# Optimization experiments

Hardware: AMD Instinct MI355X
Metric: run time of the kernel (lower is better)

The kernel has to match this reference:

```python
import jax, jax.numpy as jnp
import numpy as np

DIM = 1024
HID = 2816  # int(2*4096/3)=2730 rounded up to multiple of 256
E = 2       # n_modalities
N = 32768   # tokens
EPS = 1e-5


def setup_inputs() -> dict:
    key = jax.random.key(0)
    ks = jax.random.split(key, 6)
    x = jax.random.normal(ks[0], (N, DIM), jnp.float32)
    # per-token modality label -> disjoint boolean masks [E, N]
    labels = jax.random.randint(ks[1], (N,), 0, E)
    modality_masks = labels[None, :] == jnp.arange(E)[:, None]
    s_in = 1.0 / np.sqrt(DIM)
    s_hid = 1.0 / np.sqrt(HID)
    # nn.Linear stores weight as [out_features, in_features]
    w1 = jax.random.normal(ks[2], (E, HID, DIM), jnp.float32) * s_in
    w3 = jax.random.normal(ks[3], (E, HID, DIM), jnp.float32) * s_in
    w2 = jax.random.normal(ks[4], (E, DIM, HID), jnp.float32) * s_hid
    norm_w = jnp.ones((E, DIM), jnp.float32)
    return {"x": x, "modality_masks": modality_masks,
            "w1": w1, "w3": w3, "w2": w2, "norm_w": norm_w}


def reference(x, modality_masks, w1, w3, w2, norm_w):
    # Each expert: SwiGLU FFN followed by RMSNorm (computed in fp32).
    def expert(W1, W3, W2, g):
        h = jax.nn.silu(x @ W1.T) * (x @ W3.T)   # [N, HID]
        o = h @ W2.T                              # [N, DIM]
        of = o.astype(jnp.float32)
        n = of * jax.lax.rsqrt(jnp.mean(of * of, axis=-1, keepdims=True) + EPS)
        return (n * g.astype(jnp.float32)).astype(o.dtype)

    outs = jax.vmap(expert)(w1, w3, w2, norm_w)   # [E, N, DIM]
    merged = jnp.zeros_like(x)
    for i in range(E - 1, -1, -1):
        merged = jnp.where(modality_masks[i][:, None], outs[i], merged)
    return merged
```

## Files before the change

kernel.cpp:

```cpp
#include <hip/hip_runtime.h>
#include <stdint.h>

#define DIM   1024
#define HID   2816
#define NEXP  2
#define NTOK  32768
#define RMS_EPS 1e-5f
#define NK1   16
#define NK2   44
#define NNT1  22
#define NNT2  4

typedef unsigned short u16;
typedef unsigned int   u32;
typedef __bf16 bf16_t;
typedef bf16_t bf16x8 __attribute__((ext_vector_type(8)));
typedef float  f32x4  __attribute__((ext_vector_type(4)));
typedef float  f32x4v __attribute__((ext_vector_type(4)));

#define BAR() asm volatile("s_barrier" ::: "memory")
#define WAIT6() asm volatile("s_waitcnt vmcnt(6)" ::: "memory")
#define WAIT0() asm volatile("s_waitcnt vmcnt(0)" ::: "memory")
#define MFMA_(a,b,c) __builtin_amdgcn_mfma_f32_16x16x32_bf16(a, b, c, 0, 0, 0)

__device__ __forceinline__ u16 f2bf(float f) {
  u32 u = __float_as_uint(f);
  u += 0x7FFFu + ((u >> 16) & 1u);
  return (u16)(u >> 16);
}

__device__ __forceinline__ void gld16(void* lds, const void* g) {
  __builtin_amdgcn_global_load_lds(
      (__attribute__((address_space(1))) void*)g,
      (__attribute__((address_space(3))) void*)lds, 16, 0, 0);
}

__device__ __forceinline__ int detect_layout(const u32* mi) {
  const int lane = threadIdx.x & 63;
  bool all01 = true, allf = true;
  for (int j = 0; j < 8; ++j) {
    u32 w = mi[j * 64 + lane];
    all01 &= (w <= 1u);
    allf  &= (w == 0u || w == 0x3F800000u);
  }
  unsigned long long b01 = __ballot(all01);
  unsigned long long bfl = __ballot(allf);
  if (b01 == ~0ull) return 0;
  if (bfl == ~0ull) return 1;
  return 2;
}

__device__ __forceinline__ bool mask_at(const void* m, int layout, int e, int n) {
  if (layout == 0) return ((const u32*)m)[e * NTOK + n] != 0u;
  if (layout == 1) return ((const float*)m)[e * NTOK + n] != 0.f;
  return ((const unsigned char*)m)[e * NTOK + n] != 0;
}

__device__ __forceinline__ int label_of(const void* m, int layout, int n) {
  for (int e = 0; e < NEXP; ++e)
    if (mask_at(m, layout, e, n)) return e;
  return 0;
}

__global__ __launch_bounds__(1024) void k_setup(const void* __restrict__ masks,
                                                int* __restrict__ meta,
                                                int* __restrict__ idx) {
  const int layout = detect_layout((const u32*)masks);
  const int t = threadIdx.x;
  const int base_n = t << 5;
  u32 bits = 0; int c0 = 0;
  for (int j = 0; j < 32; ++j) {
    const int l_ = label_of(masks, layout, base_n + j);
    bits |= ((u32)l_) << j;
    c0 += 1 - l_;
  }
  int inc = c0;
#pragma unroll
  for (int d = 1; d < 64; d <<= 1) {
    int v = __shfl_up(inc, d, 64);
    if ((t & 63) >= d) inc += v;
  }
  __shared__ int wsum[16];
  __shared__ int wexc[17];
  const int wv = t >> 6;
  if ((t & 63) == 63) wsum[wv] = inc;
  __syncthreads();
  if (t == 0) {
    int a = 0;
    for (int w = 0; w < 16; ++w) { wexc[w] = a; a += wsum[w]; }
    wexc[16] = a;
  }
  __syncthreads();
  const int cnt0 = wexc[16];
  int p0 = wexc[wv] + inc - c0;
  int p1 = cnt0 + base_n - p0;
  for (int j = 0; j < 32; ++j) {
    const int n = base_n + j;
    if ((bits >> j) & 1u) idx[p1++] = n;
    else                  idx[p0++] = n;
  }
  if (t == 0) { meta[0] = cnt0; meta[1] = NTOK - cnt0; }
}

__global__ void k_cvtw(const float* __restrict__ w1, const float* __restrict__ w3,
                       const float* __restrict__ w2, u16* __restrict__ w1b,
                       u16* __restrict__ w3b, u16* __restrict__ w2b, int n4) {
  const int stride = gridDim.x * blockDim.x;
  for (int i = blockIdx.x * blockDim.x + threadIdx.x; i < 3 * n4; i += stride) {
    const f32x4v* src; ushort4* dst; int j;
    if (i < n4)            { src = (const f32x4v*)w1; dst = (ushort4*)w1b; j = i; }
    else if (i < 2 * n4)   { src = (const f32x4v*)w3; dst = (ushort4*)w3b; j = i - n4; }
    else                   { src = (const f32x4v*)w2; dst = (ushort4*)w2b; j = i - 2 * n4; }
    const f32x4v v = __builtin_nontemporal_load(&src[j]);
    ushort4 o;
    o.x = f2bf(v[0]); o.y = f2bf(v[1]); o.z = f2bf(v[2]); o.w = f2bf(v[3]);
    dst[j] = o;
  }
}

__global__ __launch_bounds__(256) void k_cvtx(const float* __restrict__ x,
                                              const int* __restrict__ idx,
                                              u16* __restrict__ xg) {
  const int r = blockIdx.x;
  const int tok = idx[r];
  const f32x4v v = __builtin_nontemporal_load(
      &((const f32x4v*)(x + ((size_t)tok << 10)))[threadIdx.x]);
  ushort4 o;
  o.x = f2bf(v[0]); o.y = f2bf(v[1]); o.z = f2bf(v[2]); o.w = f2bf(v[3]);
  ((ushort4*)(xg + ((size_t)r << 10)))[threadIdx.x] = o;
}


#define ST1A(BUF, HH, P_, KT) {                                        \
    char* _d = (char*)&sA[BUF][(HH) * 8192] + t * 16;                  \
    gld16(_d,        ((HH) ? P_.a2 : P_.a0) + (size_t)(KT) * 64);      \
    gld16(_d + 8192, ((HH) ? P_.a3 : P_.a1) + (size_t)(KT) * 64); }

#define ST1B(BUF, HH, P_, KT) {                                                 \
    gld16((char*)&sB1[BUF][(HH) * 4096] + t * 16,                               \
          ((HH) ? P_.b11 : P_.b10) + (size_t)(KT) * 64);                        \
    gld16((char*)&sB3[BUF][(HH) * 4096] + t * 16,                               \
          ((HH) ? P_.b31 : P_.b30) + (size_t)(KT) * 64); }

#define G1_PH(MQ, NQ, ...) {                                                   \
    if ((NQ) == 0) {                                                           \
      _Pragma("unroll") for (int mi = 0; mi < 4; ++mi) {                       \
        af0[mi] = *(const bf16x8*)&sAc[aBase + (MQ)*8192 + mi*1024 + kb0];     \
        af1[mi] = *(const bf16x8*)&sAc[aBase + (MQ)*8192 + mi*1024 + kb1];     \
      }                                                                        \
    }                                                                          \
    b1f0 = *(const bf16x8*)&sB1c[bBase + (NQ)*4096 + kb0];                     \
    b1f1 = *(const bf16x8*)&sB1c[bBase + (NQ)*4096 + kb1];                     \
    b3f0 = *(const bf16x8*)&sB3c[bBase + (NQ)*4096 + kb0];                     \
    b3f1 = *(const bf16x8*)&sB3c[bBase + (NQ)*4096 + kb1];                     \
    __VA_ARGS__                                                                \
    BAR();                                                                     \
    __builtin_amdgcn_s_setprio(1);                                             \
    _Pragma("unroll") for (int mi = 0; mi < 4; ++mi) {                         \
      acc1[MQ][NQ][mi] = MFMA_(af0[mi], b1f0, acc1[MQ][NQ][mi]);               \
      acc3[MQ][NQ][mi] = MFMA_(af0[mi], b3f0, acc3[MQ][NQ][mi]);               \
      acc1[MQ][NQ][mi] = MFMA_(af1[mi], b1f1, acc1[MQ][NQ][mi]);               \
      acc3[MQ][NQ][mi] = MFMA_(af1[mi], b3f1, acc3[MQ][NQ][mi]);               \
    }                                                                          \
    __builtin_amdgcn_s_setprio(0);                                             \
  }

#define SETUP1(P_, IT) {                                                        \
    int _it = (IT);                                                            \
    int _nt = _it / mcnt;                                                      \
    int _j  = _it - _nt * mcnt;                                                \
    int _m  = c + (_j << 3);                                                   \
    P_.nT   = _nt;                                                             \
    int _e  = _m >= nmt0;                                                      \
    P_.mT   = _e ? _m - nmt0 : _m;                                             \
    P_.cnt  = _e ? cnt1 : cnt0;                                                \
    P_.bas  = _e ? cnt0 : 0;                                                   \
    int _rg;                                                                   \
    _rg = P_.mT*256       + r0; _rg = _rg < P_.cnt ? _rg : P_.cnt-1;           \
    P_.a0 = xg + (size_t)(P_.bas+_rg)*DIM + srcoff;                            \
    _rg = P_.mT*256 +  64 + r0; _rg = _rg < P_.cnt ? _rg : P_.cnt-1;           \
    P_.a1 = xg + (size_t)(P_.bas+_rg)*DIM + srcoff;                            \
    _rg = P_.mT*256 + 128 + r0; _rg = _rg < P_.cnt ? _rg : P_.cnt-1;           \
    P_.a2 = xg + (size_t)(P_.bas+_rg)*DIM + srcoff;                            \
    _rg = P_.mT*256 + 192 + r0; _rg = _rg < P_.cnt ? _rg : P_.cnt-1;           \
    P_.a3 = xg + (size_t)(P_.bas+_rg)*DIM + srcoff;                            \
    size_t _o = ((size_t)_e * HID + (size_t)P_.nT * 128 + r0) * DIM + srcoff;  \
    P_.b10 = w1b + _o; P_.b11 = w1b + _o + (size_t)64 * DIM;                   \
    P_.b30 = w3b + _o; P_.b31 = w3b + _o + (size_t)64 * DIM; }

__global__ __launch_bounds__(512, 1) void k_gemm1(
    const u16* __restrict__ xg, const u16* __restrict__ w1b,
    const u16* __restrict__ w3b, const int* __restrict__ meta,
    u16* __restrict__ h)
{
  const int cnt0 = meta[0], cnt1 = meta[1];
  const int nmt0 = (cnt0 + 255) >> 8;
  const int nmt  = nmt0 + ((cnt1 + 255) >> 8);
  const int c = blockIdx.x & 7, q = blockIdx.x >> 3;
  const int mcnt  = (nmt > c) ? (((nmt - 1 - c) >> 3) + 1) : 0;
  const int items = mcnt * NNT1;
  int i = q;
  if (i >= items) return;

  __shared__ __attribute__((aligned(16))) u16 sA [2][256 * 64];
  __shared__ __attribute__((aligned(16))) u16 sB1[2][128 * 64];
  __shared__ __attribute__((aligned(16))) u16 sB3[2][128 * 64];

  const int t = threadIdx.x;
  const int srcoff = ((t & 7) ^ ((t >> 3) & 7)) * 8;
  const int r0 = t >> 3;
  const int wid = t >> 6, l = t & 63;
  const int wr = wid >> 2, wc = wid & 3;
  const int l15 = l & 15, lk = l >> 4, l7 = l & 7;
  const int kb0 = ((0 + lk) ^ l7) * 8;
  const int kb1 = ((4 + lk) ^ l7) * 8;
  const int aBase = (wr * 64 + l15) * 64;
  const int bBase = (wc * 16 + l15) * 64;

  struct P { const u16 *a0,*a1,*a2,*a3,*b10,*b11,*b30,*b31; int mT,cnt,bas,nT; };
  P cur, nxt;
  SETUP1(cur, i)
  bool hasN = (i + 32) < items;
  if (hasN) { SETUP1(nxt, i + 32) } else { nxt = cur; }

  f32x4 acc1[2][2][4] = {};
  f32x4 acc3[2][2][4] = {};
  bf16x8 af0[4], af1[4], b1f0, b1f1, b3f0, b3f1;

  ST1A(0, 0, cur, 0) ST1A(0, 1, cur, 0) ST1B(0, 0, cur, 0) ST1B(0, 1, cur, 0)
  ST1A(1, 0, cur, 1) ST1A(1, 1, cur, 1) ST1B(1, 0, cur, 1)
  WAIT6();
  BAR();

  for (;;) {
#pragma unroll 2
    for (int k = 0; k < NK1 - 2; ++k) {
      const u16* sAc  = &sA [k & 1][0];
      const u16* sB1c = &sB1[k & 1][0];
      const u16* sB3c = &sB3[k & 1][0];
      G1_PH(0, 0, ST1B((k & 1) ^ 1, 1, cur, k + 1))
      BAR();
      G1_PH(0, 1, ST1A(k & 1, 0, cur, k + 2))
      BAR();
      G1_PH(1, 0, )
      BAR();
      G1_PH(1, 1, ST1A(k & 1, 1, cur, k + 2) ST1B(k & 1, 0, cur, k + 2))
      WAIT6();
      BAR();
    }
    {
      const u16* sAc  = &sA [0][0];
      const u16* sB1c = &sB1[0][0];
      const u16* sB3c = &sB3[0][0];
      G1_PH(0, 0, ST1B(1, 1, cur, 15))
      BAR();
      G1_PH(0, 1, if (hasN) ST1A(0, 0, nxt, 0))
      BAR();
      G1_PH(1, 0, )
      BAR();
      G1_PH(1, 1, if (hasN) { ST1A(0, 1, nxt, 0) ST1B(0, 0, nxt, 0) })
      if (hasN) WAIT6(); else WAIT0();
      BAR();
    }
    {
      const u16* sAc  = &sA [1][0];
      const u16* sB1c = &sB1[1][0];
      const u16* sB3c = &sB3[1][0];
      G1_PH(0, 0, if (hasN) ST1B(0, 1, nxt, 0))
      BAR();
      G1_PH(0, 1, if (hasN) ST1A(1, 0, nxt, 1))
      BAR();
      G1_PH(1, 0, )
      BAR();
      G1_PH(1, 1, if (hasN) { ST1A(1, 1, nxt, 1) ST1B(1, 0, nxt, 1) })
      if (hasN) WAIT6();
      BAR();
    }

#pragma unroll
    for (int mq = 0; mq < 2; ++mq)
#pragma unroll
      for (int mi = 0; mi < 4; ++mi)
#pragma unroll
        for (int r = 0; r < 4; ++r) {
          const int lrow = mq * 128 + wr * 64 + mi * 16 + lk * 4 + r;
          const int rg = cur.mT * 256 + lrow;
          if (rg < cur.cnt) {
            u16* hrow = h + (size_t)(cur.bas + rg) * HID + cur.nT * 128 + wc * 16 + l15;
#pragma unroll
            for (int nq = 0; nq < 2; ++nq) {
              const float a = acc1[mq][nq][mi][r];
              const float b = acc3[mq][nq][mi][r];
              __builtin_nontemporal_store(f2bf((a / (1.f + __expf(-a))) * b),
                                          hrow + nq * 64);
            }
          }
        }

    if (!hasN) break;
    cur = nxt;
    i += 32;
    hasN = (i + 32) < items;
    if (hasN) SETUP1(nxt, i + 32)
#pragma unroll
    for (int a_ = 0; a_ < 2; ++a_)
#pragma unroll
      for (int b_ = 0; b_ < 2; ++b_)
#pragma unroll
        for (int m_ = 0; m_ < 4; ++m_) {
          acc1[a_][b_][m_] = (f32x4){0.f, 0.f, 0.f, 0.f};
          acc3[a_][b_][m_] = (f32x4){0.f, 0.f, 0.f, 0.f};
        }
  }
}


#define ST2A(BUF, HH, P_, KT) {                                        \
    char* _d = (char*)&sA[BUF][(HH) * 8192] + t * 16;                  \
    gld16(_d,        ((HH) ? P_.a2 : P_.a0) + (size_t)(KT) * 64);      \
    gld16(_d + 8192, ((HH) ? P_.a3 : P_.a1) + (size_t)(KT) * 64); }

#define ST2B(BUF, HH, P_, KT) {                                        \
    char* _d = (char*)&sB[BUF][(HH) * 8192] + t * 16;                  \
    gld16(_d,        ((HH) ? P_.b2 : P_.b0) + (size_t)(KT) * 64);      \
    gld16(_d + 8192, ((HH) ? P_.b3 : P_.b1) + (size_t)(KT) * 64); }

#define G2_PH(MQ, NQ, ...) {                                                   \
    if ((NQ) == 0) {                                                           \
      _Pragma("unroll") for (int mi = 0; mi < 4; ++mi) {                       \
        af0[mi] = *(const bf16x8*)&sAc[aBase + (MQ)*8192 + mi*1024 + kb0];     \
        af1[mi] = *(const bf16x8*)&sAc[aBase + (MQ)*8192 + mi*1024 + kb1];     \
      }                                                                        \
    }                                                                          \
    _Pragma("unroll") for (int ni = 0; ni < 2; ++ni) {                         \
      bf0[ni] = *(const bf16x8*)&sBc[bBase + (NQ)*8192 + ni*1024 + kb0];       \
      bf1[ni] = *(const bf16x8*)&sBc[bBase + (NQ)*8192 + ni*1024 + kb1];       \
    }                                                                          \
    __VA_ARGS__                                                                \
    BAR();                                                                     \
    __builtin_amdgcn_s_setprio(1);                                             \
    _Pragma("unroll") for (int mi = 0; mi < 4; ++mi)                           \
      _Pragma("unroll") for (int ni = 0; ni < 2; ++ni) {                       \
        acc[MQ][NQ][mi][ni] = MFMA_(af0[mi], bf0[ni], acc[MQ][NQ][mi][ni]);    \
        acc[MQ][NQ][mi][ni] = MFMA_(af1[mi], bf1[ni], acc[MQ][NQ][mi][ni]);    \
      }                                                                        \
    __builtin_amdgcn_s_setprio(0);                                             \
  }

#define SETUP2(P_, IT) {                                                        \
    int _it = (IT);                                                            \
    int _nt = _it / mcnt;                                                      \
    int _j  = _it - _nt * mcnt;                                                \
    int _m  = c + (_j << 3);                                                   \
    P_.nT   = _nt;                                                             \
    int _e  = _m >= nmt0;                                                      \
    P_.mT   = _e ? _m - nmt0 : _m;                                             \
    P_.cnt  = _e ? cnt1 : cnt0;                                                \
    P_.bas  = _e ? cnt0 : 0;                                                   \
    int _rg;                                                                   \
    _rg = P_.mT*256       + r0; _rg = _rg < P_.cnt ? _rg : P_.cnt-1;           \
    P_.a0 = hbuf + (size_t)(P_.bas+_rg)*HID + srcoff;                          \
    _rg = P_.mT*256 +  64 + r0; _rg = _rg < P_.cnt ? _rg : P_.cnt-1;           \
    P_.a1 = hbuf + (size_t)(P_.bas+_rg)*HID + srcoff;                          \
    _rg = P_.mT*256 + 128 + r0; _rg = _rg < P_.cnt ? _rg : P_.cnt-1;           \
    P_.a2 = hbuf + (size_t)(P_.bas+_rg)*HID + srcoff;                          \
    _rg = P_.mT*256 + 192 + r0; _rg = _rg < P_.cnt ? _rg : P_.cnt-1;           \
    P_.a3 = hbuf + (size_t)(P_.bas+_rg)*HID + srcoff;                          \
    size_t _wb = ((size_t)_e * DIM + (size_t)P_.nT * 256 + r0) * HID + srcoff; \
    P_.b0 = w2b + _wb;                                                         \
    P_.b1 = w2b + _wb + (size_t) 64 * HID;                                     \
    P_.b2 = w2b + _wb + (size_t)128 * HID;                                     \
    P_.b3 = w2b + _wb + (size_t)192 * HID; }

__global__ __launch_bounds__(512, 1) void k_gemm2(
    const u16* __restrict__ hbuf, const u16* __restrict__ w2b,
    const int* __restrict__ meta, const int* __restrict__ idx,
    float* __restrict__ out)
{
  const int cnt0 = meta[0], cnt1 = meta[1];
  const int nmt0 = (cnt0 + 255) >> 8;
  const int nmt  = nmt0 + ((cnt1 + 255) >> 8);
  const int c = blockIdx.x & 7, q = blockIdx.x >> 3;
  const int mcnt  = (nmt > c) ? (((nmt - 1 - c) >> 3) + 1) : 0;
  const int items = mcnt * NNT2;
  int i = q;
  if (i >= items) return;

  __shared__ __attribute__((aligned(16))) u16 sA[2][256 * 64];
  __shared__ __attribute__((aligned(16))) u16 sB[2][256 * 64];

  const int t = threadIdx.x;
  const int srcoff = ((t & 7) ^ ((t >> 3) & 7)) * 8;
  const int r0 = t >> 3;
  const int wid = t >> 6, l = t & 63;
  const int wr = wid >> 2, wc = wid & 3;
  const int l15 = l & 15, lk = l >> 4, l7 = l & 7;
  const int kb0 = ((0 + lk) ^ l7) * 8;
  const int kb1 = ((4 + lk) ^ l7) * 8;
  const int aBase = (wr * 64 + l15) * 64;
  const int bBase = (wc * 32 + l15) * 64;

  struct P { const u16 *a0,*a1,*a2,*a3,*b0,*b1,*b2,*b3; int mT,cnt,bas,nT; };
  P cur, nxt;
  SETUP2(cur, i)
  bool hasN = (i + 32) < items;
  if (hasN) { SETUP2(nxt, i + 32) } else { nxt = cur; }

  f32x4 acc[2][2][4][2] = {};
  bf16x8 af0[4], af1[4], bf0[2], bf1[2];

  ST2A(0, 0, cur, 0) ST2A(0, 1, cur, 0) ST2B(0, 0, cur, 0) ST2B(0, 1, cur, 0)
  ST2A(1, 0, cur, 1) ST2A(1, 1, cur, 1) ST2B(1, 0, cur, 1)
  WAIT6();
  BAR();

  for (;;) {
#pragma unroll 2
    for (int k = 0; k < NK2 - 2; ++k) {
      const u16* sAc = &sA[k & 1][0];
      const u16* sBc = &sB[k & 1][0];
      G2_PH(0, 0, ST2B((k & 1) ^ 1, 1, cur, k + 1))
      BAR();
      G2_PH(0, 1, ST2A(k & 1, 0, cur, k + 2))
      BAR();
      G2_PH(1, 0, )
      BAR();
      G2_PH(1, 1, ST2A(k & 1, 1, cur, k + 2) ST2B(k & 1, 0, cur, k + 2))
      WAIT6();
      BAR();
    }
    {
      const u16* sAc = &sA[0][0];
      const u16* sBc = &sB[0][0];
      G2_PH(0, 0, ST2B(1, 1, cur, NK2 - 1))
      BAR();
      G2_PH(0, 1, if (hasN) ST2A(0, 0, nxt, 0))
      BAR();
      G2_PH(1, 0, )
      BAR();
      G2_PH(1, 1, if (hasN) { ST2A(0, 1, nxt, 0) ST2B(0, 0, nxt, 0) })
      if (hasN) WAIT6(); else WAIT0();
      BAR();
    }
    {
      const u16* sAc = &sA[1][0];
      const u16* sBc = &sB[1][0];
      G2_PH(0, 0, if (hasN) ST2B(0, 1, nxt, 0))
      BAR();
      G2_PH(0, 1, if (hasN) ST2A(1, 0, nxt, 1))
      BAR();
      G2_PH(1, 0, )
      BAR();
      G2_PH(1, 1, if (hasN) { ST2A(1, 1, nxt, 1) ST2B(1, 0, nxt, 1) })
      if (hasN) WAIT6();
      BAR();
    }

#pragma unroll
    for (int mq = 0; mq < 2; ++mq)
#pragma unroll
      for (int mi = 0; mi < 4; ++mi)
#pragma unroll
        for (int r = 0; r < 4; ++r) {
          const int lrow = mq * 128 + wr * 64 + mi * 16 + lk * 4 + r;
          const int rg = cur.mT * 256 + lrow;
          if (rg < cur.cnt) {
            const int tok = idx[cur.bas + rg];
            float* orow = out + (size_t)tok * DIM + cur.nT * 256 + wc * 32 + l15;
#pragma unroll
            for (int nq = 0; nq < 2; ++nq)
#pragma unroll
              for (int ni = 0; ni < 2; ++ni)
                orow[nq * 128 + ni * 16] = acc[mq][nq][mi][ni][r];
          }
        }

    if (!hasN) break;
    cur = nxt;
    i += 32;
    hasN = (i + 32) < items;
    if (hasN) SETUP2(nxt, i + 32)
#pragma unroll
    for (int a_ = 0; a_ < 2; ++a_)
#pragma unroll
      for (int b_ = 0; b_ < 2; ++b_)
#pragma unroll
        for (int m_ = 0; m_ < 4; ++m_)
#pragma unroll
          for (int n_ = 0; n_ < 2; ++n_)
            acc[a_][b_][m_][n_] = (f32x4){0.f, 0.f, 0.f, 0.f};
  }
}

__global__ __launch_bounds__(256) void k_rms(
    float* __restrict__ out, const float* __restrict__ nw,
    const int* __restrict__ meta, const int* __restrict__ idx)
{
  const int wv = threadIdx.x >> 6, ln = threadIdx.x & 63;
  const int r = blockIdx.x * 4 + wv;
  const int e = (r >= meta[0]) ? 1 : 0;
  const int tok = idx[r];
  float* row = out + (size_t)tok * DIM;
  const float* g = nw + (size_t)e * DIM;

  float4 v[4];
  float ss = 0.f;
#pragma unroll
  for (int p = 0; p < 4; ++p) {
    v[p] = ((const float4*)row)[p * 64 + ln];
    ss += v[p].x * v[p].x + v[p].y * v[p].y + v[p].z * v[p].z + v[p].w * v[p].w;
  }
#pragma unroll
  for (int off = 32; off; off >>= 1) ss += __shfl_xor(ss, off, 64);
  const float sc = rsqrtf(ss * (1.0f / DIM) + RMS_EPS);
#pragma unroll
  for (int p = 0; p < 4; ++p) {
    const float4 gg = ((const float4*)g)[p * 64 + ln];
    v[p].x *= sc * gg.x; v[p].y *= sc * gg.y;
    v[p].z *= sc * gg.z; v[p].w *= sc * gg.w;
    ((float4*)row)[p * 64 + ln] = v[p];
  }
}

extern "C" void kernel_launch(void* const* d_in, const int* in_sizes, int n_in,
                              void* d_out, int out_size, void* d_ws, size_t ws_size,
                              hipStream_t stream)
{
  const float* x     = (const float*)d_in[0];
  const void*  masks = d_in[1];
  const float* w1    = (const float*)d_in[2];
  const float* w3    = (const float*)d_in[3];
  const float* w2    = (const float*)d_in[4];
  const float* nw    = (const float*)d_in[5];
  float* out = (float*)d_out;

  char* ws = (char*)d_ws;
  constexpr size_t OFF_IDX = 256;
  constexpr size_t OFF_XB  = OFF_IDX + (size_t)NTOK * 4;
  constexpr size_t OFF_W1B = OFF_XB + (size_t)NTOK * DIM * 2;
  constexpr size_t SZ_W    = (size_t)NEXP * HID * DIM * 2;
  constexpr size_t OFF_W3B = OFF_W1B + SZ_W;
  constexpr size_t OFF_W2B = OFF_W3B + SZ_W;
  constexpr size_t OFF_H   = OFF_W2B + SZ_W;

  int* meta = (int*)ws;
  int* idx  = (int*)(ws + OFF_IDX);
  u16* xg   = (u16*)(ws + OFF_XB);
  u16* w1b  = (u16*)(ws + OFF_W1B);
  u16* w3b  = (u16*)(ws + OFF_W3B);
  u16* w2b  = (u16*)(ws + OFF_W2B);
  u16* h    = (u16*)(ws + OFF_H);

  k_setup<<<1, 1024, 0, stream>>>(masks, meta, idx);

  const int wn4 = NEXP * HID * DIM / 4;
  k_cvtw<<<2048, 256, 0, stream>>>(w1, w3, w2, w1b, w3b, w2b, wn4);
  k_cvtx<<<NTOK, 256, 0, stream>>>(x, idx, xg);

  k_gemm1<<<256, 512, 0, stream>>>(xg, w1b, w3b, meta, h);
  k_gemm2<<<256, 512, 0, stream>>>(h, w2b, meta, idx, out);
  k_rms<<<NTOK / 4, 256, 0, stream>>>(out, nw, meta, idx);
}
```

Before: 783.5 us.

## Merge mask setup into weight conversion and give GEMM blocks contiguous tile ranges

Folds the single-block mask scan/prefix-sum kernel into the weight-conversion kernel as block 0, removing one launch and letting the scan overlap the conversion. In both GEMMs each block now processes a contiguous chunk of work items instead of a stride-32 sequence. In GEMM2, SETUP2 changes its index decode so consecutive items cycle through the N tiles for a fixed M tile. The intent is for consecutive items to share the A tile (or the same weight panel) in cache, at the risk of uneven load balance across blocks.

```diff
diff --git a/kernel.cpp b/kernel.cpp
--- a/kernel.cpp
+++ b/kernel.cpp
@@ -62,51 +62,52 @@
   return 0;
 }
 
-__global__ __launch_bounds__(1024) void k_setup(const void* __restrict__ masks,
-                                                int* __restrict__ meta,
-                                                int* __restrict__ idx) {
-  const int layout = detect_layout((const u32*)masks);
+__global__ __launch_bounds__(1024) void k_prep(
+    const void* __restrict__ masks, int* __restrict__ meta, int* __restrict__ idx,
+    const float* __restrict__ w1, const float* __restrict__ w3,
+    const float* __restrict__ w2, u16* __restrict__ w1b,
+    u16* __restrict__ w3b, u16* __restrict__ w2b, int n4)
+{
   const int t = threadIdx.x;
-  const int base_n = t << 5;
-  u32 bits = 0; int c0 = 0;
-  for (int j = 0; j < 32; ++j) {
-    const int l_ = label_of(masks, layout, base_n + j);
-    bits |= ((u32)l_) << j;
-    c0 += 1 - l_;
-  }
-  int inc = c0;
-#pragma unroll
-  for (int d = 1; d < 64; d <<= 1) {
-    int v = __shfl_up(inc, d, 64);
-    if ((t & 63) >= d) inc += v;
-  }
-  __shared__ int wsum[16];
-  __shared__ int wexc[17];
-  const int wv = t >> 6;
-  if ((t & 63) == 63) wsum[wv] = inc;
-  __syncthreads();
-  if (t == 0) {
-    int a = 0;
-    for (int w = 0; w < 16; ++w) { wexc[w] = a; a += wsum[w]; }
-    wexc[16] = a;
-  }
-  __syncthreads();
-  const int cnt0 = wexc[16];
-  int p0 = wexc[wv] + inc - c0;
-  int p1 = cnt0 + base_n - p0;
-  for (int j = 0; j < 32; ++j) {
-    const int n = base_n + j;
-    if ((bits >> j) & 1u) idx[p1++] = n;
-    else                  idx[p0++] = n;
-  }
-  if (t == 0) { meta[0] = cnt0; meta[1] = NTOK - cnt0; }
-}
-
-__global__ void k_cvtw(const float* __restrict__ w1, const float* __restrict__ w3,
-                       const float* __restrict__ w2, u16* __restrict__ w1b,
-                       u16* __restrict__ w3b, u16* __restrict__ w2b, int n4) {
-  const int stride = gridDim.x * blockDim.x;
-  for (int i = blockIdx.x * blockDim.x + threadIdx.x; i < 3 * n4; i += stride) {
+  if (blockIdx.x == 0) {
+    const int layout = detect_layout((const u32*)masks);
+    const int base_n = t << 5;
+    u32 bits = 0; int c0 = 0;
+    for (int j = 0; j < 32; ++j) {
+      const int l_ = label_of(masks, layout, base_n + j);
+      bits |= ((u32)l_) << j;
+      c0 += 1 - l_;
+    }
+    int inc = c0;
+#pragma unroll
+    for (int d = 1; d < 64; d <<= 1) {
+      int v = __shfl_up(inc, d, 64);
+      if ((t & 63) >= d) inc += v;
+    }
+    __shared__ int wsum[16];
+    __shared__ int wexc[17];
+    const int wv = t >> 6;
+    if ((t & 63) == 63) wsum[wv] = inc;
+    __syncthreads();
+    if (t == 0) {
+      int a = 0;
+      for (int w = 0; w < 16; ++w) { wexc[w] = a; a += wsum[w]; }
+      wexc[16] = a;
+    }
+    __syncthreads();
+    const int cnt0 = wexc[16];
+    int p0 = wexc[wv] + inc - c0;
+    int p1 = cnt0 + base_n - p0;
+    for (int j = 0; j < 32; ++j) {
+      const int n = base_n + j;
+      if ((bits >> j) & 1u) idx[p1++] = n;
+      else                  idx[p0++] = n;
+    }
+    if (t == 0) { meta[0] = cnt0; meta[1] = NTOK - cnt0; }
+    return;
+  }
+  const int stride = (gridDim.x - 1) * blockDim.x;
+  for (int i = (blockIdx.x - 1) * blockDim.x + t; i < 3 * n4; i += stride) {
     const f32x4v* src; ushort4* dst; int j;
     if (i < n4)            { src = (const f32x4v*)w1; dst = (ushort4*)w1b; j = i; }
     else if (i < 2 * n4)   { src = (const f32x4v*)w3; dst = (ushort4*)w3b; j = i - n4; }
@@ -199,8 +200,10 @@
   const int c = blockIdx.x & 7, q = blockIdx.x >> 3;
   const int mcnt  = (nmt > c) ? (((nmt - 1 - c) >> 3) + 1) : 0;
   const int items = mcnt * NNT1;
-  int i = q;
-  if (i >= items) return;
+  const int ipb   = (items + 31) >> 5;
+  int i = q * ipb;
+  const int hi = (i + ipb < items) ? (i + ipb) : items;
+  if (i >= hi) return;
 
   __shared__ __attribute__((aligned(16))) u16 sA [2][256 * 64];
   __shared__ __attribute__((aligned(16))) u16 sB1[2][128 * 64];
@@ -220,8 +223,8 @@
   struct P { const u16 *a0,*a1,*a2,*a3,*b10,*b11,*b30,*b31; int mT,cnt,bas,nT; };
   P cur, nxt;
   SETUP1(cur, i)
-  bool hasN = (i + 32) < items;
-  if (hasN) { SETUP1(nxt, i + 32) } else { nxt = cur; }
+  bool hasN = (i + 1) < hi;
+  if (hasN) { SETUP1(nxt, i + 1) } else { nxt = cur; }
 
   f32x4 acc1[2][2][4] = {};
   f32x4 acc3[2][2][4] = {};
@@ -299,9 +302,9 @@
 
     if (!hasN) break;
     cur = nxt;
-    i += 32;
-    hasN = (i + 32) < items;
-    if (hasN) SETUP1(nxt, i + 32)
+    i += 1;
+    hasN = (i + 1) < hi;
+    if (hasN) SETUP1(nxt, i + 1)
 #pragma unroll
     for (int a_ = 0; a_ < 2; ++a_)
 #pragma unroll
@@ -349,10 +352,9 @@
 
 #define SETUP2(P_, IT) {                                                        \
     int _it = (IT);                                                            \
-    int _nt = _it / mcnt;                                                      \
-    int _j  = _it - _nt * mcnt;                                                \
+    P_.nT   = _it & 3;                                                         \
+    int _j  = _it >> 2;                                                        \
     int _m  = c + (_j << 3);                                                   \
-    P_.nT   = _nt;                                                             \
     int _e  = _m >= nmt0;                                                      \
     P_.mT   = _e ? _m - nmt0 : _m;                                             \
     P_.cnt  = _e ? cnt1 : cnt0;                                                \
@@ -383,8 +385,10 @@
   const int c = blockIdx.x & 7, q = blockIdx.x >> 3;
   const int mcnt  = (nmt > c) ? (((nmt - 1 - c) >> 3) + 1) : 0;
   const int items = mcnt * NNT2;
-  int i = q;
-  if (i >= items) return;
+  const int ipb   = (items + 31) >> 5;
+  int i = q * ipb;
+  const int hi = (i + ipb < items) ? (i + ipb) : items;
+  if (i >= hi) return;
 
   __shared__ __attribute__((aligned(16))) u16 sA[2][256 * 64];
   __shared__ __attribute__((aligned(16))) u16 sB[2][256 * 64];
@@ -403,8 +407,8 @@
   struct P { const u16 *a0,*a1,*a2,*a3,*b0,*b1,*b2,*b3; int mT,cnt,bas,nT; };
   P cur, nxt;
   SETUP2(cur, i)
-  bool hasN = (i + 32) < items;
-  if (hasN) { SETUP2(nxt, i + 32) } else { nxt = cur; }
+  bool hasN = (i + 1) < hi;
+  if (hasN) { SETUP2(nxt, i + 1) } else { nxt = cur; }
 
   f32x4 acc[2][2][4][2] = {};
   bf16x8 af0[4], af1[4], bf0[2], bf1[2];
@@ -477,9 +481,9 @@
 
     if (!hasN) break;
     cur = nxt;
-    i += 32;
-    hasN = (i + 32) < items;
-    if (hasN) SETUP2(nxt, i + 32)
+    i += 1;
+    hasN = (i + 1) < hi;
+    if (hasN) SETUP2(nxt, i + 1)
 #pragma unroll
     for (int a_ = 0; a_ < 2; ++a_)
 #pragma unroll
@@ -551,10 +555,9 @@
   u16* w2b  = (u16*)(ws + OFF_W2B);
   u16* h    = (u16*)(ws + OFF_H);
 
-  k_setup<<<1, 1024, 0, stream>>>(masks, meta, idx);
-
   const int wn4 = NEXP * HID * DIM / 4;
-  k_cvtw<<<2048, 256, 0, stream>>>(w1, w3, w2, w1b, w3b, w2b, wn4);
+  k_prep<<<1025, 1024, 0, stream>>>(masks, meta, idx, w1, w3, w2,
+                                    w1b, w3b, w2b, wn4);
   k_cvtx<<<NTOK, 256, 0, stream>>>(x, idx, xg);
 
   k_gemm1<<<256, 512, 0, stream>>>(xg, w1b, w3b, meta, h);
```

Result: slower. 820.7 us (+4.7%).
